# Optimization experiments

Hardware: AMD Instinct MI355X
Metric: run time of the kernel (lower is better)

Reference implementation:

```python
import jax, jax.numpy as jnp
import numpy as np

V = 36      # nodes per graph (3 temporal x 12 spatial)
C = 3       # temporal embedding slots
S = 12      # spatial embedding slots
F0 = 1025   # input feature width
H1, H2 = 256, 64
B = 1024    # graphs
N = B * V
DEG = 8     # random in-block neighbors per node (symmetrized -> 16 avg degree)
BN_EPS = 1e-5


def _edges(k):
    # 8 random neighbors per node within its own 36-node block, symmetrized
    nbr = jax.random.randint(k, (N, DEG), 0, V)
    block = (jnp.arange(N) // V) * V
    dst = (nbr + block[:, None]).reshape(-1)
    src = jnp.repeat(jnp.arange(N), DEG)
    return jnp.stack([jnp.concatenate([src, dst]),
                      jnp.concatenate([dst, src])]).astype(jnp.int32)


def setup_inputs() -> dict:
    k = jax.random.split(jax.random.key(0), 40)
    lin = lambda kk, i, o: (jax.random.normal(kk, (i, o), jnp.float32) / np.sqrt(i)).astype(jnp.float32)
    d = {}
    d['xF'] = jax.random.normal(k[0], (N, F0), jnp.float32)
    d['xD'] = jax.random.normal(k[1], (N, F0), jnp.float32)
    d['edge_index_F'] = _edges(k[2])
    d['edge_index_D'] = _edges(k[3])
    d['TembF'] = jax.random.normal(k[4], (C, F0), jnp.float32)
    d['SembF'] = jax.random.normal(k[5], (S, F0), jnp.float32)
    d['TembD'] = jax.random.normal(k[6], (C, F0), jnp.float32)
    d['SembD'] = jax.random.normal(k[7], (S, F0), jnp.float32)
    # ChebConv K=2 weights (Theta_0, Theta_1), biases; BatchNorm gamma/beta
    d['W0F1'] = lin(k[8], F0, H1); d['W1F1'] = lin(k[9], F0, H1); d['bF1'] = jnp.zeros((H1,), jnp.float32)
    d['gF1'] = jnp.ones((H1,), jnp.float32); d['btF1'] = jnp.zeros((H1,), jnp.float32)
    d['W0F2'] = lin(k[10], H1, H2); d['W1F2'] = lin(k[11], H1, H2); d['bF2'] = jnp.zeros((H2,), jnp.float32)
    d['gF2'] = jnp.ones((H2,), jnp.float32); d['btF2'] = jnp.zeros((H2,), jnp.float32)
    d['W0D1'] = lin(k[12], F0, H1); d['W1D1'] = lin(k[13], F0, H1); d['bD1'] = jnp.zeros((H1,), jnp.float32)
    d['gD1'] = jnp.ones((H1,), jnp.float32); d['btD1'] = jnp.zeros((H1,), jnp.float32)
    d['W0D2'] = lin(k[14], H1, H2); d['W1D2'] = lin(k[15], H1, H2); d['bD2'] = jnp.zeros((H2,), jnp.float32)
    d['gD2'] = jnp.ones((H2,), jnp.float32); d['btD2'] = jnp.zeros((H2,), jnp.float32)
    # fusion linear [256->5]; branch heads are tied-at-init clones of its halves
    Wlin = lin(k[16], 2 * (2 * H2), 5)
    blin = jnp.zeros((5,), jnp.float32)
    d['WlinF'] = Wlin[:2 * H2, :]; d['blinF'] = blin
    d['WlinD'] = Wlin[2 * H2:, :]; d['blinD'] = blin
    d['Wlin'] = Wlin; d['blin'] = blin
    return d


def _cheb(x, ei, W0, W1, b):
    # PyG ChebConv K=2, sym norm, lambda_max=2: out = x@W0 + (L_hat x)@W1 + b,
    # L_hat = -D^{-1/2} A D^{-1/2}. Transform-then-aggregate (linear, cheaper).
    n = x.shape[0]
    src, dst = ei[0], ei[1]
    deg = jax.ops.segment_sum(jnp.ones(src.shape, jnp.float32), src, n)
    dinv = jnp.where(deg > 0, jax.lax.rsqrt(jnp.maximum(deg, 1.0)), 0.0)
    w = -(dinv[src] * dinv[dst])                       # [E]
    h1 = x @ W1                                        # [N, out]
    tx1 = jax.ops.segment_sum(w[:, None] * h1[src], dst, n)  # scatter-add
    return x @ W0 + tx1 + b


def _bn_relu(x, g, bt):
    mu = x.mean(0)
    var = x.var(0)  # biased, as torch BatchNorm1d training-mode normalization
    return jax.nn.relu((x - mu) * jax.lax.rsqrt(var + BN_EPS) * g + bt)


def _branch(x, ei, Temb, Semb, W0a, W1a, ba, ga, bta, W0b, W1b, bb, gb, btb):
    n = x.shape[0]
    bsz = n // V
    x = x.reshape(bsz, C, S, F0).transpose(0, 2, 1, 3)      # [B,12,3,1025]
    x = x + Temb[None, None, :, :] + Semb[None, :, None, :]
    x = x.transpose(0, 2, 1, 3).reshape(n, F0)
    x = _bn_relu(_cheb(x, ei, W0a, W1a, ba), ga, bta)
    x = _bn_relu(_cheb(x, ei, W0b, W1b, bb), gb, btb)        # [N,64]
    # rows 12..23 of each 36-node block, pooled per graph
    idx = (jnp.arange(bsz)[:, None] * V + S + jnp.arange(S)[None, :]).reshape(-1)
    seg = jnp.repeat(jnp.arange(bsz), S)
    xs = x[idx]
    mx = jax.ops.segment_max(xs, seg, bsz)
    mn = jax.ops.segment_sum(xs, seg, bsz) / float(S)
    return jnp.concatenate([mx, mn], axis=1)                 # [B,128]


def reference(xF, xD, edge_index_F, edge_index_D, TembF, SembF, TembD, SembD,
              W0F1, W1F1, bF1, gF1, btF1, W0F2, W1F2, bF2, gF2, btF2,
              W0D1, W1D1, bD1, gD1, btD1, W0D2, W1D2, bD2, gD2, btD2,
              WlinF, blinF, WlinD, blinD, Wlin, blin):
    featF = _branch(xF, edge_index_F, TembF, SembF, W0F1, W1F1, bF1, gF1, btF1,
                    W0F2, W1F2, bF2, gF2, btF2)
    featD = _branch(xD, edge_index_D, TembD, SembD, W0D1, W1D1, bD1, gD1, btD1,
                    W0D2, W1D2, bD2, gD2, btD2)
    outF = jax.nn.softmax(featF @ WlinF + blinF, axis=-1)
    outD = jax.nn.softmax(featD @ WlinD + blinD, axis=-1)
    fusion = jnp.concatenate([featF, featD], axis=1)
    out = jax.nn.softmax(fusion @ Wlin + blin, axis=-1)
    return (outF, outD, fusion, out)
```

## Files before the change

kernel.cpp:

```cpp
#include <hip/hip_runtime.h>
#include <math.h>

#define NN    36864
#define F0    1025
#define H1D   256
#define H2D   64
#define VV    36
#define SS    12
#define BSZ   1024
#define BN_EPS 1e-5f

#define KT1   17
#define EMB_LD 1088
#define WT1_STRIDE  ((size_t)4*17*8192)
#define WT2_STRIDE  ((size_t)4*8192)

typedef __bf16 bf16x8 __attribute__((ext_vector_type(8)));
typedef __bf16 bf16x4 __attribute__((ext_vector_type(4)));
typedef float  f32x4  __attribute__((ext_vector_type(4)));

__device__ __forceinline__ float4 ld4u(const float* p) {
    float4 v;
    __builtin_memcpy(&v, p, 16);
    return v;
}

__global__ void k_zero(float* __restrict__ p, int n) {
    int i = blockIdx.x * blockDim.x + threadIdx.x;
    if (i < n) p[i] = 0.f;
}

__global__ void k_deginit(float* __restrict__ degAll) {
    int br = blockIdx.y;
    int i = blockIdx.x * 256 + threadIdx.x;
    if (i < NN) degAll[(size_t)br * NN + i] = 8.f;
}

__global__ void k_deg(const int* __restrict__ eiF, const int* __restrict__ eiD,
                      int Eh, float* __restrict__ degAll) {
    int br = blockIdx.y;
    const int* src = (br ? eiD : eiF) + Eh;
    float* deg = degAll + (size_t)br * NN;
    int e = blockIdx.x * blockDim.x + threadIdx.x;
    if (e < Eh) atomicAdd(&deg[src[e]], 1.f);
}

__device__ __forceinline__ float dinv_f(float d) {
    return d > 0.f ? rsqrtf(fmaxf(d, 1.f)) : 0.f;
}

__global__ void k_scatter(const int* __restrict__ eiF, const int* __restrict__ eiD,
                          int E, const float* __restrict__ degAll, float* __restrict__ AdjAll) {
    int br = blockIdx.y;
    const int* src = br ? eiD : eiF;
    const int* dst = src + E;
    const float* deg = degAll + (size_t)br * NN;
    float* Adj = AdjAll + (size_t)br * BSZ * (VV * VV);
    int e = blockIdx.x * blockDim.x + threadIdx.x;
    if (e >= E) return;
    int s = src[e], d = dst[e];
    float w = -dinv_f(deg[s]) * dinv_f(deg[d]);
    int blk = s / VV;
    atomicAdd(&Adj[(size_t)blk * (VV * VV) + (d - blk * VV) * VV + (s - blk * VV)], w);
}

__global__ __launch_bounds__(256) void k_prepEmb(
    const float* __restrict__ TembF, const float* __restrict__ SembF,
    const float* __restrict__ TembD, const float* __restrict__ SembD,
    float* __restrict__ embSAll) {
    int br = blockIdx.y;
    const float* Temb = br ? TembD : TembF;
    const float* Semb = br ? SembD : SembF;
    float* out = embSAll + (size_t)br * VV * EMB_LD;
    int id = blockIdx.x * 256 + threadIdx.x;
    if (id >= VV * (EMB_LD / 4)) return;
    int lv = id / (EMB_LD / 4);
    int k0 = (id - lv * (EMB_LD / 4)) * 4;
    const float* pt = Temb + (size_t)(lv / SS) * F0;
    const float* ps = Semb + (size_t)(lv % SS) * F0;
    float4 v;
    float* vp = (float*)&v;
#pragma unroll
    for (int j = 0; j < 4; ++j) {
        int k = k0 + j;
        vp[j] = (k < F0) ? (pt[k] + ps[k]) : 0.f;
    }
    *reinterpret_cast<float4*>(out + (size_t)lv * EMB_LD + k0) = v;
}

__global__ __launch_bounds__(256) void k_prepW(
    const float* __restrict__ WaF, const float* __restrict__ WbF,
    const float* __restrict__ WaD, const float* __restrict__ WbD,
    __bf16* __restrict__ Wt, int K, int nkt, int split, int ldw, size_t brStride) {
    int br = blockIdx.y;
    const float* Wa = br ? WaD : WaF;
    const float* Wb = br ? WbD : WbF;
    __bf16* out = Wt + (size_t)br * brStride;

    int id = blockIdx.x * 256 + threadIdx.x;
    int gpc = nkt * 8;
    int c = id / gpc, gi = id - c * gpc;
    int kt = gi >> 3, g = gi & 7;
    int k0 = kt * 64 + g * 8;
    const float* src = (c < split) ? (Wa + c) : (Wb + (c - split));
    bf16x8 ov;
#pragma unroll
    for (int j = 0; j < 8; ++j) {
        int k = k0 + j;
        float v = (k < K) ? src[(size_t)k * ldw] : 0.f;
        ov[j] = (__bf16)v;
    }
    int r = c & 127, bn = c >> 7;
    size_t dst = ((size_t)(bn * nkt + kt) << 13) + r * 64 + ((g ^ (r & 7)) << 3);
    *(bf16x8*)(out + dst) = ov;
}

__global__ __launch_bounds__(512) void k_gemm1f(
    const float* __restrict__ xF, const float* __restrict__ xD,
    const float* __restrict__ embSAll,
    const __bf16* __restrict__ Wt1All,
    __bf16* __restrict__ H0All, __bf16* __restrict__ H1All) {
    __shared__ __align__(16) __bf16 As[2 * 8192];
    __shared__ __align__(16) __bf16 Bs[2 * 16384];
    const int tid = threadIdx.x;
    const int lane = tid & 63, wid = tid >> 6;

    const int flat = blockIdx.x;
    const int w = (flat & 7) * 144 + (flat >> 3);
    const int cy = w & 1;
    const int t2 = w >> 1;
    const int bm = t2 % 288;
    const int br = t2 / 288;

    const float* x    = br ? xD : xF;
    const float* embS = embSAll + (size_t)br * VV * EMB_LD;
    const __bf16* Wt = Wt1All + (size_t)br * WT1_STRIDE;
    __bf16* H0 = H0All + (size_t)br * NN * H1D;
    __bf16* H1 = H1All + (size_t)br * NN * H1D;

    const int wr = wid >> 2, wc = wid & 3;
    const int l15 = lane & 15, lg = lane >> 4;
    const int bn0 = cy * 2;

    const int kc = (lane & 15) * 4;
    const float *px[4], *pe[4];
    int dso[4];
#pragma unroll
    for (int i = 0; i < 4; ++i) {
        int r = wid * 16 + i * 4 + (lane >> 4);
        int g = bm * 128 + r;
        int lv = g % VV;
        px[i] = x + (size_t)g * F0 + kc;
        pe[i] = embS + (size_t)lv * EMB_LD + kc;
        dso[i] = r * 64 + (((kc >> 3) ^ (r & 7)) << 3) + (kc & 4);
    }

    int offA[2][4], offB[2][4];
#pragma unroll
    for (int kk = 0; kk < 2; ++kk) {
#pragma unroll
        for (int m = 0; m < 4; ++m) {
            int rowA = wr * 64 + m * 16 + l15;
            offA[kk][m] = rowA * 64 + (((kk * 4 + lg) ^ (rowA & 7)) << 3);
        }
#pragma unroll
        for (int n = 0; n < 4; ++n) {
            int col = wc * 64 + n * 16 + l15;
            offB[kk][n] = (col >> 7) * 8192 + (col & 127) * 64
                          + (((kk * 4 + lg) ^ (col & 7)) << 3);
        }
    }

    f32x4 acc[4][4];
#pragma unroll
    for (int m = 0; m < 4; ++m)
#pragma unroll
        for (int n = 0; n < 4; ++n) acc[m][n] = (f32x4){0.f, 0.f, 0.f, 0.f};

    f32x4 xa0[4], xa1[4];

    auto issueX = [&](int kt, f32x4 (&xa)[4]) {
        int ko = kt * 64, kb = ko + kc;
#pragma unroll
        for (int i = 0; i < 4; ++i) {
            if (kb + 3 < F0) {
                float4 a = ld4u(px[i] + ko);
                xa[i] = (f32x4){a.x, a.y, a.z, a.w};
            } else {
                f32x4 v = {0.f, 0.f, 0.f, 0.f};
#pragma unroll
                for (int j = 0; j < 4; ++j)
                    if (kb + j < F0) v[j] = px[i][ko + j];
                xa[i] = v;
            }
        }
    };
    auto writeA = [&](int kt, int buf, f32x4 (&xa)[4]) {
        int ko = kt * 64;
#pragma unroll
        for (int i = 0; i < 4; ++i) {
            float4 e = *reinterpret_cast<const float4*>(pe[i] + ko);
            bf16x4 wv;
            wv[0] = (__bf16)(xa[i][0] + e.x);
            wv[1] = (__bf16)(xa[i][1] + e.y);
            wv[2] = (__bf16)(xa[i][2] + e.z);
            wv[3] = (__bf16)(xa[i][3] + e.w);
            *(bf16x4*)(As + buf * 8192 + dso[i]) = wv;
        }
    };
    auto issueB = [&](int kt, int buf) {
#pragma unroll
        for (int cc = 0; cc < 4; ++cc) {
            int q = (wid * 4 + cc) * 512;
            int h = q >> 13, qi = q & 8191;
            const __bf16* src = Wt + (((size_t)(bn0 + h) * KT1 + kt) << 13)
                                + qi + (lane << 3);
            __builtin_amdgcn_global_load_lds(
                (const __attribute__((address_space(1))) void*)src,
                (__attribute__((address_space(3))) void*)(Bs + buf * 16384 + q), 16, 0, 0);
        }
    };
    auto mfmaStep = [&](int cur) {
        const __bf16* Ab = As + cur * 8192;
        const __bf16* Bb = Bs + cur * 16384;
#pragma unroll
        for (int kk = 0; kk < 2; ++kk) {
            bf16x8 af[4], bb[4];
#pragma unroll
            for (int m = 0; m < 4; ++m) af[m] = *(const bf16x8*)(Ab + offA[kk][m]);
#pragma unroll
            for (int n = 0; n < 4; ++n) bb[n] = *(const bf16x8*)(Bb + offB[kk][n]);
#pragma unroll
            for (int m = 0; m < 4; ++m)
#pragma unroll
                for (int n = 0; n < 4; ++n)
                    acc[m][n] = __builtin_amdgcn_mfma_f32_16x16x32_bf16(
                        af[m], bb[n], acc[m][n], 0, 0, 0);
        }
    };

    issueX(0, xa0);
    issueB(0, 0);
    writeA(0, 0, xa0);
    issueX(1, xa1);

    for (int kt = 0; kt < KT1; kt += 2) {
        __syncthreads();
        if (kt + 1 < KT1) issueB(kt + 1, 1);
        if (kt + 2 < KT1) issueX(kt + 2, xa0);
        mfmaStep(0);
        if (kt + 1 < KT1) writeA(kt + 1, 1, xa1);
        if (kt + 1 >= KT1) break;
        __syncthreads();
        if (kt + 2 < KT1) issueB(kt + 2, 0);
        if (kt + 3 < KT1) issueX(kt + 3, xa1);
        mfmaStep(1);
        if (kt + 2 < KT1) writeA(kt + 2, 0, xa0);
    }

    const int cr = lg * 4;
#pragma unroll
    for (int m = 0; m < 4; ++m) {
        int grow = bm * 128 + wr * 64 + m * 16 + cr;
#pragma unroll
        for (int n = 0; n < 4; ++n) {
            int gc = cy * 256 + wc * 64 + n * 16 + l15;
#pragma unroll
            for (int j = 0; j < 4; ++j) {
                int r = grow + j;
                if (gc < 256) H0[(size_t)r * H1D + gc] = (__bf16)acc[m][n][j];
                else          H1[(size_t)r * H1D + (gc - 256)] = (__bf16)acc[m][n][j];
            }
        }
    }
}

__global__ __launch_bounds__(256, 2) void k_gemm2f(
    const __bf16* __restrict__ YAll, const float* __restrict__ coefAll,
    const __bf16* __restrict__ Wt2All,
    float* __restrict__ G0All, __bf16* __restrict__ G1All) {
    __shared__ __align__(16) __bf16 As[2 * 8192];
    __shared__ __align__(16) __bf16 Bs[2 * 8192];
    const int tid = threadIdx.x;
    const int lane = tid & 63, wid = tid >> 6;
    const int bm = blockIdx.x, br = blockIdx.z;
    const __bf16* Y   = YAll + (size_t)br * NN * H1D;
    const float* coef = coefAll + (size_t)br * 2 * H1D;
    const __bf16* Wt  = Wt2All + (size_t)br * WT2_STRIDE;
    float*  G0 = G0All + (size_t)br * NN * H2D;
    __bf16* G1 = G1All + (size_t)br * NN * H2D;

    const int wr = wid >> 1, wc = wid & 1;
    const int l15 = lane & 15, lg = lane >> 4;

    const int kc = (lane & 15) * 4;
    const __bf16* pyr[8];
    int dso[8];
#pragma unroll
    for (int i = 0; i < 8; ++i) {
        int r = wid * 32 + i * 4 + (lane >> 4);
        pyr[i] = Y + (size_t)(bm * 128 + r) * H1D + kc;
        dso[i] = r * 64 + (((kc >> 3) ^ (r & 7)) << 3) + (kc & 4);
    }

    int offA[2][4], offB[2][4];
#pragma unroll
    for (int kk = 0; kk < 2; ++kk)
#pragma unroll
        for (int m = 0; m < 4; ++m) {
            int rowA = wr * 64 + m * 16 + l15;
            offA[kk][m] = rowA * 64 + (((kk * 4 + lg) ^ (rowA & 7)) << 3);
            int col = wc * 64 + m * 16 + l15;
            offB[kk][m] = col * 64 + (((kk * 4 + lg) ^ (col & 7)) << 3);
        }

    f32x4 acc[4][4];
#pragma unroll
    for (int m = 0; m < 4; ++m)
#pragma unroll
        for (int n = 0; n < 4; ++n) acc[m][n] = (f32x4){0.f, 0.f, 0.f, 0.f};

    bf16x4 ya[8];

    auto issueY = [&](int kt) {
        int k0 = kt * 64;
#pragma unroll
        for (int i = 0; i < 8; ++i)
            ya[i] = *reinterpret_cast<const bf16x4*>(pyr[i] + k0);
    };
    auto writeA = [&](int kt, int buf) {
        int k0 = kt * 64;
        float4 cA = *reinterpret_cast<const float4*>(coef + k0 + kc);
        float4 cB = *reinterpret_cast<const float4*>(coef + H1D + k0 + kc);
#pragma unroll
        for (int i = 0; i < 8; ++i) {
            bf16x4 wv;
            wv[0] = (__bf16)fmaxf(fmaf((float)ya[i][0], cA.x, cB.x), 0.f);
            wv[1] = (__bf16)fmaxf(fmaf((float)ya[i][1], cA.y, cB.y), 0.f);
            wv[2] = (__bf16)fmaxf(fmaf((float)ya[i][2], cA.z, cB.z), 0.f);
            wv[3] = (__bf16)fmaxf(fmaf((float)ya[i][3], cA.w, cB.w), 0.f);
            *(bf16x4*)(As + buf * 8192 + dso[i]) = wv;
        }
    };
    auto issueB = [&](int kt, int buf) {
#pragma unroll
        for (int cc = 0; cc < 4; ++cc) {
            int q = (wid * 4 + cc) * 512;
            const __bf16* src = Wt + ((size_t)kt << 13) + q + (lane << 3);
            __builtin_amdgcn_global_load_lds(
                (const __attribute__((address_space(1))) void*)src,
                (__attribute__((address_space(3))) void*)(Bs + buf * 8192 + q), 16, 0, 0);
        }
    };

    issueB(0, 0);
    issueY(0);
    writeA(0, 0);

    for (int kt = 0; kt < 4; ++kt) {
        const int cur = kt & 1, nxt = cur ^ 1;
        __syncthreads();
        if (kt + 1 < 4) {
            issueB(kt + 1, nxt);
            issueY(kt + 1);
        }
        const __bf16* Ab = As + cur * 8192;
        const __bf16* Bb = Bs + cur * 8192;
#pragma unroll
        for (int kk = 0; kk < 2; ++kk) {
            bf16x8 af[4], bb[4];
#pragma unroll
            for (int m = 0; m < 4; ++m) af[m] = *(const bf16x8*)(Ab + offA[kk][m]);
#pragma unroll
            for (int n = 0; n < 4; ++n) bb[n] = *(const bf16x8*)(Bb + offB[kk][n]);
#pragma unroll
            for (int m = 0; m < 4; ++m)
#pragma unroll
                for (int n = 0; n < 4; ++n)
                    acc[m][n] = __builtin_amdgcn_mfma_f32_16x16x32_bf16(
                        af[m], bb[n], acc[m][n], 0, 0, 0);
        }
        if (kt + 1 < 4) writeA(kt + 1, nxt);
    }

    const int cr = lg * 4;
#pragma unroll
    for (int m = 0; m < 4; ++m) {
        int grow = bm * 128 + wr * 64 + m * 16 + cr;
#pragma unroll
        for (int n = 0; n < 4; ++n) {
            int col = wc * 64 + n * 16 + l15;
#pragma unroll
            for (int j = 0; j < 4; ++j) {
                int r = grow + j;
                if (col < 64) G0[(size_t)r * H2D + col] = acc[m][n][j];
                else          G1[(size_t)r * H2D + (col - 64)] = (__bf16)acc[m][n][j];
            }
        }
    }
}

__global__ __launch_bounds__(256) void k_combine_stats1(
    const float* __restrict__ AdjAll, const __bf16* __restrict__ H1All,
    const float* __restrict__ bF, const float* __restrict__ bD,
    __bf16* __restrict__ YAll, float* __restrict__ stAll) {
    __shared__ float Adj_s[VV * VV];
    __shared__ float red[256 * 9];
    int b = blockIdx.x, br = blockIdx.y, t = threadIdx.x;
    const float* Adj = AdjAll + ((size_t)br * BSZ + b) * (VV * VV);
    const __bf16* h1 = H1All + ((size_t)br * NN + (size_t)b * VV) * H1D;
    __bf16* yb = YAll + ((size_t)br * NN + (size_t)b * VV) * H1D;
    float* st = stAll + (size_t)br * 2 * H1D;
    const float* bias = br ? bD : bF;

    for (int e = t; e < VV * VV; e += 256) Adj_s[e] = Adj[e];
    __syncthreads();

    int c0 = (t & 63) * 4, r0 = t >> 6;
    float4 bv = *reinterpret_cast<const float4*>(bias + c0);
    float acc[9][4];
#pragma unroll
    for (int i = 0; i < 9; ++i) {
        bf16x4 y = *reinterpret_cast<const bf16x4*>(yb + (size_t)(r0 + 4 * i) * H1D + c0);
        acc[i][0] = (float)y[0] + bv.x; acc[i][1] = (float)y[1] + bv.y;
        acc[i][2] = (float)y[2] + bv.z; acc[i][3] = (float)y[3] + bv.w;
    }
#pragma unroll 4
    for (int j = 0; j < VV; ++j) {
        bf16x4 hv = *reinterpret_cast<const bf16x4*>(h1 + (size_t)j * H1D + c0);
        float h0 = (float)hv[0], h1f = (float)hv[1], h2 = (float)hv[2], h3 = (float)hv[3];
#pragma unroll
        for (int i = 0; i < 9; ++i) {
            float a = Adj_s[(r0 + 4 * i) * VV + j];
            acc[i][0] = fmaf(a, h0, acc[i][0]);
            acc[i][1] = fmaf(a, h1f, acc[i][1]);
            acc[i][2] = fmaf(a, h2, acc[i][2]);
            acc[i][3] = fmaf(a, h3, acc[i][3]);
        }
    }
    float s[4] = {0, 0, 0, 0}, s2[4] = {0, 0, 0, 0};
#pragma unroll
    for (int i = 0; i < 9; ++i) {
        bf16x4 wv;
        wv[0] = (__bf16)acc[i][0]; wv[1] = (__bf16)acc[i][1];
        wv[2] = (__bf16)acc[i][2]; wv[3] = (__bf16)acc[i][3];
        *reinterpret_cast<bf16x4*>(yb + (size_t)(r0 + 4 * i) * H1D + c0) = wv;
#pragma unroll
        for (int k = 0; k < 4; ++k) { s[k] += acc[i][k]; s2[k] += acc[i][k] * acc[i][k]; }
    }
#pragma unroll
    for (int k = 0; k < 4; ++k) { red[t * 9 + k] = s[k]; red[t * 9 + 4 + k] = s2[k]; }
    __syncthreads();
    {
        int cg = t >> 2, k = t & 3;
        float ss = 0.f, ss2 = 0.f;
#pragma unroll
        for (int q = 0; q < 4; ++q) {
            ss  += red[(q * 64 + cg) * 9 + k];
            ss2 += red[(q * 64 + cg) * 9 + 4 + k];
        }
        atomicAdd(&st[t], ss);
        atomicAdd(&st[H1D + t], ss2);
    }
}

__global__ __launch_bounds__(256) void k_combine_stats2(
    const float* __restrict__ AdjAll, const __bf16* __restrict__ G1All,
    const float* __restrict__ bF, const float* __restrict__ bD,
    float* __restrict__ YAll, float* __restrict__ stAll) {
    __shared__ float Adj_s[VV * VV];
    __shared__ float red[256 * 9];
    int b = blockIdx.x, br = blockIdx.y, t = threadIdx.x;
    const float* Adj = AdjAll + ((size_t)br * BSZ + b) * (VV * VV);
    const __bf16* g1 = G1All + ((size_t)br * NN + (size_t)b * VV) * H2D;
    float* yb = YAll + ((size_t)br * NN + (size_t)b * VV) * H2D;
    float* st = stAll + (size_t)br * 2 * H2D;
    const float* bias = br ? bD : bF;

    for (int e = t; e < VV * VV; e += 256) Adj_s[e] = Adj[e];
    __syncthreads();

    int c0 = (t & 15) * 4, r0 = t >> 4;
    int nr = (r0 < 4) ? 3 : 2;
    float4 bv = *reinterpret_cast<const float4*>(bias + c0);
    float acc[3][4];
    for (int i = 0; i < nr; ++i) {
        float4 y = *reinterpret_cast<const float4*>(yb + (size_t)(r0 + 16 * i) * H2D + c0);
        acc[i][0] = y.x + bv.x; acc[i][1] = y.y + bv.y;
        acc[i][2] = y.z + bv.z; acc[i][3] = y.w + bv.w;
    }
#pragma unroll 4
    for (int j = 0; j < VV; ++j) {
        bf16x4 hv = *reinterpret_cast<const bf16x4*>(g1 + (size_t)j * H2D + c0);
        float h0 = (float)hv[0], h1f = (float)hv[1], h2 = (float)hv[2], h3 = (float)hv[3];
        for (int i = 0; i < nr; ++i) {
            float a = Adj_s[(r0 + 16 * i) * VV + j];
            acc[i][0] = fmaf(a, h0, acc[i][0]);
            acc[i][1] = fmaf(a, h1f, acc[i][1]);
            acc[i][2] = fmaf(a, h2, acc[i][2]);
            acc[i][3] = fmaf(a, h3, acc[i][3]);
        }
    }
    float s[4] = {0, 0, 0, 0}, s2[4] = {0, 0, 0, 0};
    for (int i = 0; i < nr; ++i) {
        *reinterpret_cast<float4*>(yb + (size_t)(r0 + 16 * i) * H2D + c0) =
            make_float4(acc[i][0], acc[i][1], acc[i][2], acc[i][3]);
#pragma unroll
        for (int k = 0; k < 4; ++k) { s[k] += acc[i][k]; s2[k] += acc[i][k] * acc[i][k]; }
    }
#pragma unroll
    for (int k = 0; k < 4; ++k) { red[t * 9 + k] = s[k]; red[t * 9 + 4 + k] = s2[k]; }
    __syncthreads();
    if (t < 2 * H2D) {
        int cg = (t & 63) >> 2, k = t & 3, which = t >> 6;
        float ss = 0.f;
#pragma unroll
        for (int q = 0; q < 16; ++q) ss += red[(q * 16 + cg) * 9 + which * 4 + k];
        atomicAdd(&st[(t >> 6) * H2D + (t & 63)], ss);
    }
}

__global__ void k_fin(const float* __restrict__ stAll,
                      const float* __restrict__ gF, const float* __restrict__ btF,
                      const float* __restrict__ gD, const float* __restrict__ btD,
                      float* __restrict__ coefAll, int H) {
    int br = blockIdx.x, t = threadIdx.x;
    const float* st = stAll + (size_t)br * 2 * H;
    float* coef = coefAll + (size_t)br * 2 * H;
    const float* g = br ? gD : gF;
    const float* bt = br ? btD : btF;
    if (t >= H) return;
    float mu = st[t] / (float)NN;
    float var = st[H + t] / (float)NN - mu * mu;
    float sA = g[t] * rsqrtf(var + BN_EPS);
    coef[t] = sA;
    coef[H + t] = bt[t] - mu * sA;
}

__global__ __launch_bounds__(64) void k_pool(const float* __restrict__ Y2All,
                                             const float* __restrict__ coefAll,
                                             float* __restrict__ featF,
                                             float* __restrict__ featD) {
    int b = blockIdx.x, br = blockIdx.y, c = threadIdx.x;
    const float* Y2 = Y2All + (size_t)br * NN * H2D;
    const float* coef = coefAll + (size_t)br * 2 * H2D;
    float* feat = br ? featD : featF;
    float sA = coef[c], sB = coef[H2D + c];
    float mx = -1e30f, sm = 0.f;
    const float* yb = Y2 + ((size_t)b * VV + SS) * H2D + c;
#pragma unroll
    for (int i = 0; i < SS; ++i) {
        float v = fmaxf(fmaf(yb[i * H2D], sA, sB), 0.f);
        mx = fmaxf(mx, v);
        sm += v;
    }
    feat[b * 128 + c] = mx;
    feat[b * 128 + 64 + c] = sm * (1.f / 12.f);
}

__global__ __launch_bounds__(128) void k_heads(
    const float* __restrict__ featF, const float* __restrict__ featD,
    const float* __restrict__ WlinF, const float* __restrict__ blinF,
    const float* __restrict__ WlinD, const float* __restrict__ blinD,
    const float* __restrict__ Wlin, const float* __restrict__ blin,
    float* __restrict__ out) {
    __shared__ float sF[128], sD[128], lg[24];
    int r = blockIdx.x, t = threadIdx.x;
    sF[t] = featF[r * 128 + t];
    sD[t] = featD[r * 128 + t];
    __syncthreads();
    float* fus = out + 10240 + (size_t)r * 256;
    fus[t] = sF[t];
    fus[128 + t] = sD[t];
    if (t < 5) {
        float a = blinF[t];
        for (int k = 0; k < 128; ++k) a += sF[k] * WlinF[k * 5 + t];
        lg[t] = a;
    } else if (t >= 8 && t < 13) {
        int j = t - 8;
        float a = blinD[j];
        for (int k = 0; k < 128; ++k) a += sD[k] * WlinD[k * 5 + j];
        lg[8 + j] = a;
    } else if (t >= 16 && t < 21) {
        int j = t - 16;
        float a = blin[j];
        for (int k = 0; k < 128; ++k) a += sF[k] * Wlin[k * 5 + j];
        for (int k = 0; k < 128; ++k) a += sD[k] * Wlin[(128 + k) * 5 + j];
        lg[16 + j] = a;
    }
    __syncthreads();
    if (t < 15) {
        int grp = t / 5, j = t % 5;
        const float* l = &lg[grp * 8];
        float m = l[0];
#pragma unroll
        for (int k = 1; k < 5; ++k) m = fmaxf(m, l[k]);
        float den = 0.f;
#pragma unroll
        for (int k = 0; k < 5; ++k) den += expf(l[k] - m);
        float v = expf(l[j] - m) / den;
        float* dst = (grp == 0) ? out : (grp == 1 ? out + 5120 : out + 272384);
        dst[r * 5 + j] = v;
    }
}

extern "C" void kernel_launch(void* const* d_in, const int* in_sizes, int n_in,
                              void* d_out, int out_size, void* d_ws, size_t ws_size,
                              hipStream_t stream) {
    const float* xF    = (const float*)d_in[0];
    const float* xD    = (const float*)d_in[1];
    const int*   eiF   = (const int*)d_in[2];
    const int*   eiD   = (const int*)d_in[3];
    const float* TembF = (const float*)d_in[4];
    const float* SembF = (const float*)d_in[5];
    const float* TembD = (const float*)d_in[6];
    const float* SembD = (const float*)d_in[7];
    const float* W0F1  = (const float*)d_in[8];
    const float* W1F1  = (const float*)d_in[9];
    const float* bF1   = (const float*)d_in[10];
    const float* gF1   = (const float*)d_in[11];
    const float* btF1  = (const float*)d_in[12];
    const float* W0F2  = (const float*)d_in[13];
    const float* W1F2  = (const float*)d_in[14];
    const float* bF2   = (const float*)d_in[15];
    const float* gF2   = (const float*)d_in[16];
    const float* btF2  = (const float*)d_in[17];
    const float* W0D1  = (const float*)d_in[18];
    const float* W1D1  = (const float*)d_in[19];
    const float* bD1   = (const float*)d_in[20];
    const float* gD1   = (const float*)d_in[21];
    const float* btD1  = (const float*)d_in[22];
    const float* W0D2  = (const float*)d_in[23];
    const float* W1D2  = (const float*)d_in[24];
    const float* bD2   = (const float*)d_in[25];
    const float* gD2   = (const float*)d_in[26];
    const float* btD2  = (const float*)d_in[27];
    const float* WlinF = (const float*)d_in[28];
    const float* blinF = (const float*)d_in[29];
    const float* WlinD = (const float*)d_in[30];
    const float* blinD = (const float*)d_in[31];
    const float* Wlin  = (const float*)d_in[32];
    const float* blin  = (const float*)d_in[33];

    const int E = in_sizes[2] / 2;

    float* ws = (float*)d_ws;
    size_t o = 0;
    __bf16* H0bf = (__bf16*)(ws + o);   o += (size_t)2 * NN * H1D / 2;
    __bf16* H1bf = (__bf16*)(ws + o);   o += (size_t)2 * NN * H1D / 2;
    float*  G0   = ws + o;              o += (size_t)2 * NN * H2D;
    __bf16* G1bf = (__bf16*)(ws + o);   o += (size_t)2 * NN * H2D / 2;
    __bf16* Wt1  = (__bf16*)(ws + o);   o += (size_t)2 * WT1_STRIDE / 2;
    __bf16* Wt2  = (__bf16*)(ws + o);   o += (size_t)2 * WT2_STRIDE / 2;
    float*  embS = ws + o;              o += (size_t)2 * VV * EMB_LD;
    float*  Adj  = ws + o;              o += (size_t)2 * BSZ * VV * VV;
    float*  st1  = ws + o;              o += 2 * 2 * H1D;
    float*  st2  = ws + o;              o += 2 * 2 * H2D;
    float*  deg  = ws + o;              o += (size_t)2 * NN;
    float*  coef1 = ws + o;             o += 2 * 2 * H1D;
    float*  coef2 = ws + o;             o += 2 * 2 * H2D;
    float*  featF = ws + o;             o += (size_t)BSZ * 128;
    float*  featD = ws + o;             o += (size_t)BSZ * 128;

    const int zeroN = 2 * (BSZ * VV * VV + 2 * H1D + 2 * H2D);

    k_zero<<<(zeroN + 255) / 256, 256, 0, stream>>>(Adj, zeroN);
    k_deginit<<<dim3(144, 2), 256, 0, stream>>>(deg);
    k_deg<<<dim3((E / 2 + 255) / 256, 2), 256, 0, stream>>>(eiF, eiD, E / 2, deg);
    k_scatter<<<dim3((E + 255) / 256, 2), 256, 0, stream>>>(eiF, eiD, E, deg, Adj);
    k_prepEmb<<<dim3(39, 2), 256, 0, stream>>>(TembF, SembF, TembD, SembD, embS);
    k_prepW<<<dim3(272, 2), 256, 0, stream>>>(W0F1, W1F1, W0D1, W1D1, Wt1,
                                              F0, 17, 256, H1D, WT1_STRIDE);
    k_prepW<<<dim3(16, 2), 256, 0, stream>>>(W0F2, W1F2, W0D2, W1D2, Wt2,
                                             H1D, 4, 64, H2D, WT2_STRIDE);
    k_gemm1f<<<dim3(1152), 512, 0, stream>>>(xF, xD, embS, Wt1, H0bf, H1bf);
    k_combine_stats1<<<dim3(BSZ, 2), 256, 0, stream>>>(Adj, H1bf, bF1, bD1, H0bf, st1);
    k_fin<<<dim3(2), 256, 0, stream>>>(st1, gF1, btF1, gD1, btD1, coef1, H1D);
    k_gemm2f<<<dim3(288, 1, 2), 256, 0, stream>>>(H0bf, coef1, Wt2, G0, G1bf);
    k_combine_stats2<<<dim3(BSZ, 2), 256, 0, stream>>>(Adj, G1bf, bF2, bD2, G0, st2);
    k_fin<<<dim3(2), 64, 0, stream>>>(st2, gF2, btF2, gD2, btD2, coef2, H2D);
    k_pool<<<dim3(BSZ, 2), 64, 0, stream>>>(G0, coef2, featF, featD);
    k_heads<<<BSZ, 128, 0, stream>>>(featF, featD, WlinF, blinF, WlinD, blinD,
                                     Wlin, blin, (float*)d_out);
}
```

Before: 445.1 us.

## Retile first GEMM to 128x128 tiles with K=32 steps and smaller LDS

```diff
diff --git a/kernel.cpp b/kernel.cpp
--- a/kernel.cpp
+++ b/kernel.cpp
@@ -10,9 +10,9 @@
 #define BSZ   1024
 #define BN_EPS 1e-5f
 
-#define KT1   17
+#define KT32  34
 #define EMB_LD 1088
-#define WT1_STRIDE  ((size_t)4*17*8192)
+#define WT1_STRIDE  ((size_t)4*34*4096)
 #define WT2_STRIDE  ((size_t)4*8192)
 
 typedef __bf16 bf16x8 __attribute__((ext_vector_type(8)));
@@ -115,60 +115,78 @@
     *(bf16x8*)(out + dst) = ov;
 }
 
-__global__ __launch_bounds__(512) void k_gemm1f(
+__global__ __launch_bounds__(256) void k_prepW32(
+    const float* __restrict__ WaF, const float* __restrict__ WbF,
+    const float* __restrict__ WaD, const float* __restrict__ WbD,
+    __bf16* __restrict__ Wt) {
+    int br = blockIdx.y;
+    const float* Wa = br ? WaD : WaF;
+    const float* Wb = br ? WbD : WbF;
+    __bf16* out = Wt + (size_t)br * WT1_STRIDE;
+
+    int id = blockIdx.x * 256 + threadIdx.x;
+    int c = id / 136, gi = id - c * 136;
+    int kt = gi >> 2, g = gi & 3;
+    int k0 = kt * 32 + g * 8;
+    const float* src = (c < 256) ? (Wa + c) : (Wb + (c - 256));
+    bf16x8 ov;
+#pragma unroll
+    for (int j = 0; j < 8; ++j) {
+        int k = k0 + j;
+        float v = (k < F0) ? src[(size_t)k * H1D] : 0.f;
+        ov[j] = (__bf16)v;
+    }
+    int r = c & 127, bn = c >> 7;
+    size_t dst = ((size_t)(bn * KT32 + kt) << 12) + r * 32 + ((g ^ ((r >> 1) & 3)) << 3);
+    *(bf16x8*)(out + dst) = ov;
+}
+
+__global__ __launch_bounds__(256, 3) void k_gemm1f(
     const float* __restrict__ xF, const float* __restrict__ xD,
     const float* __restrict__ embSAll,
     const __bf16* __restrict__ Wt1All,
     __bf16* __restrict__ H0All, __bf16* __restrict__ H1All) {
-    __shared__ __align__(16) __bf16 As[2 * 8192];
-    __shared__ __align__(16) __bf16 Bs[2 * 16384];
+    __shared__ __align__(16) __bf16 As[2 * 4096];
+    __shared__ __align__(16) __bf16 Bs[2 * 4096];
     const int tid = threadIdx.x;
     const int lane = tid & 63, wid = tid >> 6;
 
     const int flat = blockIdx.x;
-    const int w = (flat & 7) * 144 + (flat >> 3);
-    const int cy = w & 1;
-    const int t2 = w >> 1;
+    const int w = (flat & 7) * 288 + (flat >> 3);
+    const int cy = w & 3;
+    const int t2 = w >> 2;
     const int bm = t2 % 288;
     const int br = t2 / 288;
 
     const float* x    = br ? xD : xF;
     const float* embS = embSAll + (size_t)br * VV * EMB_LD;
-    const __bf16* Wt = Wt1All + (size_t)br * WT1_STRIDE;
+    const __bf16* WtT = Wt1All + (size_t)br * WT1_STRIDE + ((size_t)(cy * KT32) << 12);
     __bf16* H0 = H0All + (size_t)br * NN * H1D;
     __bf16* H1 = H1All + (size_t)br * NN * H1D;
 
-    const int wr = wid >> 2, wc = wid & 3;
+    const int wr = wid >> 1, wc = wid & 1;
     const int l15 = lane & 15, lg = lane >> 4;
-    const int bn0 = cy * 2;
-
-    const int kc = (lane & 15) * 4;
+
+    const int kc = (lane & 7) * 4;
     const float *px[4], *pe[4];
     int dso[4];
 #pragma unroll
     for (int i = 0; i < 4; ++i) {
-        int r = wid * 16 + i * 4 + (lane >> 4);
+        int r = wid * 32 + i * 8 + (lane >> 3);
         int g = bm * 128 + r;
         int lv = g % VV;
         px[i] = x + (size_t)g * F0 + kc;
         pe[i] = embS + (size_t)lv * EMB_LD + kc;
-        dso[i] = r * 64 + (((kc >> 3) ^ (r & 7)) << 3) + (kc & 4);
-    }
-
-    int offA[2][4], offB[2][4];
-#pragma unroll
-    for (int kk = 0; kk < 2; ++kk) {
-#pragma unroll
-        for (int m = 0; m < 4; ++m) {
-            int rowA = wr * 64 + m * 16 + l15;
-            offA[kk][m] = rowA * 64 + (((kk * 4 + lg) ^ (rowA & 7)) << 3);
-        }
-#pragma unroll
-        for (int n = 0; n < 4; ++n) {
-            int col = wc * 64 + n * 16 + l15;
-            offB[kk][n] = (col >> 7) * 8192 + (col & 127) * 64
-                          + (((kk * 4 + lg) ^ (col & 7)) << 3);
-        }
+        dso[i] = r * 32 + ((((kc >> 3) ^ ((r >> 1) & 3)) << 3) + (kc & 4));
+    }
+
+    int offA[4], offB[4];
+#pragma unroll
+    for (int m = 0; m < 4; ++m) {
+        int rowA = wr * 64 + m * 16 + l15;
+        offA[m] = rowA * 32 + ((lg ^ ((rowA >> 1) & 3)) << 3);
+        int col = wc * 64 + m * 16 + l15;
+        offB[m] = col * 32 + ((lg ^ ((col >> 1) & 3)) << 3);
     }
 
     f32x4 acc[4][4];
@@ -180,7 +198,7 @@
     f32x4 xa0[4], xa1[4];
 
     auto issueX = [&](int kt, f32x4 (&xa)[4]) {
-        int ko = kt * 64, kb = ko + kc;
+        int ko = kt * 32, kb = ko + kc;
 #pragma unroll
         for (int i = 0; i < 4; ++i) {
             if (kb + 3 < F0) {
@@ -196,7 +214,7 @@
         }
     };
     auto writeA = [&](int kt, int buf, f32x4 (&xa)[4]) {
-        int ko = kt * 64;
+        int ko = kt * 32;
 #pragma unroll
         for (int i = 0; i < 4; ++i) {
             float4 e = *reinterpret_cast<const float4*>(pe[i] + ko);
@@ -205,38 +223,33 @@
             wv[1] = (__bf16)(xa[i][1] + e.y);
             wv[2] = (__bf16)(xa[i][2] + e.z);
             wv[3] = (__bf16)(xa[i][3] + e.w);
-            *(bf16x4*)(As + buf * 8192 + dso[i]) = wv;
+            *(bf16x4*)(As + buf * 4096 + dso[i]) = wv;
         }
     };
     auto issueB = [&](int kt, int buf) {
 #pragma unroll
-        for (int cc = 0; cc < 4; ++cc) {
-            int q = (wid * 4 + cc) * 512;
-            int h = q >> 13, qi = q & 8191;
-            const __bf16* src = Wt + (((size_t)(bn0 + h) * KT1 + kt) << 13)
-                                + qi + (lane << 3);
+        for (int cc = 0; cc < 2; ++cc) {
+            int q = (wid * 2 + cc) * 512;
+            const __bf16* src = WtT + ((size_t)kt << 12) + q + (lane << 3);
             __builtin_amdgcn_global_load_lds(
                 (const __attribute__((address_space(1))) void*)src,
-                (__attribute__((address_space(3))) void*)(Bs + buf * 16384 + q), 16, 0, 0);
+                (__attribute__((address_space(3))) void*)(Bs + buf * 4096 + q), 16, 0, 0);
         }
     };
     auto mfmaStep = [&](int cur) {
-        const __bf16* Ab = As + cur * 8192;
-        const __bf16* Bb = Bs + cur * 16384;
-#pragma unroll
-        for (int kk = 0; kk < 2; ++kk) {
-            bf16x8 af[4], bb[4];
-#pragma unroll
-            for (int m = 0; m < 4; ++m) af[m] = *(const bf16x8*)(Ab + offA[kk][m]);
-#pragma unroll
-            for (int n = 0; n < 4; ++n) bb[n] = *(const bf16x8*)(Bb + offB[kk][n]);
-#pragma unroll
-            for (int m = 0; m < 4; ++m)
-#pragma unroll
-                for (int n = 0; n < 4; ++n)
-                    acc[m][n] = __builtin_amdgcn_mfma_f32_16x16x32_bf16(
-                        af[m], bb[n], acc[m][n], 0, 0, 0);
-        }
+        const __bf16* Ab = As + cur * 4096;
+        const __bf16* Bb = Bs + cur * 4096;
+        bf16x8 af[4], bb[4];
+#pragma unroll
+        for (int m = 0; m < 4; ++m) af[m] = *(const bf16x8*)(Ab + offA[m]);
+#pragma unroll
+        for (int n = 0; n < 4; ++n) bb[n] = *(const bf16x8*)(Bb + offB[n]);
+#pragma unroll
+        for (int m = 0; m < 4; ++m)
+#pragma unroll
+            for (int n = 0; n < 4; ++n)
+                acc[m][n] = __builtin_amdgcn_mfma_f32_16x16x32_bf16(
+                    af[m], bb[n], acc[m][n], 0, 0, 0);
     };
 
     issueX(0, xa0);
@@ -244,18 +257,18 @@
     writeA(0, 0, xa0);
     issueX(1, xa1);
 
-    for (int kt = 0; kt < KT1; kt += 2) {
+    for (int kt = 0; kt < KT32; kt += 2) {
         __syncthreads();
-        if (kt + 1 < KT1) issueB(kt + 1, 1);
-        if (kt + 2 < KT1) issueX(kt + 2, xa0);
+        if (kt + 1 < KT32) issueB(kt + 1, 1);
+        if (kt + 2 < KT32) issueX(kt + 2, xa0);
         mfmaStep(0);
-        if (kt + 1 < KT1) writeA(kt + 1, 1, xa1);
-        if (kt + 1 >= KT1) break;
+        if (kt + 1 < KT32) writeA(kt + 1, 1, xa1);
+        if (kt + 1 >= KT32) break;
         __syncthreads();
-        if (kt + 2 < KT1) issueB(kt + 2, 0);
-        if (kt + 3 < KT1) issueX(kt + 3, xa1);
+        if (kt + 2 < KT32) issueB(kt + 2, 0);
+        if (kt + 3 < KT32) issueX(kt + 3, xa1);
         mfmaStep(1);
-        if (kt + 2 < KT1) writeA(kt + 2, 0, xa0);
+        if (kt + 2 < KT32) writeA(kt + 2, 0, xa0);
     }
 
     const int cr = lg * 4;
@@ -264,7 +277,7 @@
         int grow = bm * 128 + wr * 64 + m * 16 + cr;
 #pragma unroll
         for (int n = 0; n < 4; ++n) {
-            int gc = cy * 256 + wc * 64 + n * 16 + l15;
+            int gc = cy * 128 + wc * 64 + n * 16 + l15;
 #pragma unroll
             for (int j = 0; j < 4; ++j) {
                 int r = grow + j;
@@ -669,11 +682,10 @@
     k_deg<<<dim3((E / 2 + 255) / 256, 2), 256, 0, stream>>>(eiF, eiD, E / 2, deg);
     k_scatter<<<dim3((E + 255) / 256, 2), 256, 0, stream>>>(eiF, eiD, E, deg, Adj);
     k_prepEmb<<<dim3(39, 2), 256, 0, stream>>>(TembF, SembF, TembD, SembD, embS);
-    k_prepW<<<dim3(272, 2), 256, 0, stream>>>(W0F1, W1F1, W0D1, W1D1, Wt1,
-                                              F0, 17, 256, H1D, WT1_STRIDE);
+    k_prepW32<<<dim3(272, 2), 256, 0, stream>>>(W0F1, W1F1, W0D1, W1D1, Wt1);
     k_prepW<<<dim3(16, 2), 256, 0, stream>>>(W0F2, W1F2, W0D2, W1D2, Wt2,
                                              H1D, 4, 64, H2D, WT2_STRIDE);
-    k_gemm1f<<<dim3(1152), 512, 0, stream>>>(xF, xD, embS, Wt1, H0bf, H1bf);
+    k_gemm1f<<<dim3(2304), 256, 0, stream>>>(xF, xD, embS, Wt1, H0bf, H1bf);
     k_combine_stats1<<<dim3(BSZ, 2), 256, 0, stream>>>(Adj, H1bf, bF1, bD1, H0bf, st1);
     k_fin<<<dim3(2), 256, 0, stream>>>(st1, gF1, btF1, gD1, btD1, coef1, H1D);
     k_gemm2f<<<dim3(288, 1, 2), 256, 0, stream>>>(H0bf, coef1, Wt2, G0, G1bf);
```

New measurement: 579.6 us. 1.3x slower.

## Build per-graph adjacency in shared memory and fuse pooling into heads

Applied to the files above, without the earlier changes.

```diff
diff --git a/kernel.cpp b/kernel.cpp
--- a/kernel.cpp
+++ b/kernel.cpp
@@ -30,38 +30,40 @@
     if (i < n) p[i] = 0.f;
 }
 
-__global__ void k_deginit(float* __restrict__ degAll) {
-    int br = blockIdx.y;
-    int i = blockIdx.x * 256 + threadIdx.x;
-    if (i < NN) degAll[(size_t)br * NN + i] = 8.f;
-}
-
-__global__ void k_deg(const int* __restrict__ eiF, const int* __restrict__ eiD,
-                      int Eh, float* __restrict__ degAll) {
-    int br = blockIdx.y;
-    const int* src = (br ? eiD : eiF) + Eh;
-    float* deg = degAll + (size_t)br * NN;
-    int e = blockIdx.x * blockDim.x + threadIdx.x;
-    if (e < Eh) atomicAdd(&deg[src[e]], 1.f);
-}
-
 __device__ __forceinline__ float dinv_f(float d) {
     return d > 0.f ? rsqrtf(fmaxf(d, 1.f)) : 0.f;
 }
 
-__global__ void k_scatter(const int* __restrict__ eiF, const int* __restrict__ eiD,
-                          int E, const float* __restrict__ degAll, float* __restrict__ AdjAll) {
-    int br = blockIdx.y;
-    const int* src = br ? eiD : eiF;
-    const int* dst = src + E;
-    const float* deg = degAll + (size_t)br * NN;
-    float* Adj = AdjAll + (size_t)br * BSZ * (VV * VV);
-    int e = blockIdx.x * blockDim.x + threadIdx.x;
-    if (e >= E) return;
-    int s = src[e], d = dst[e];
-    float w = -dinv_f(deg[s]) * dinv_f(deg[d]);
-    int blk = s / VV;
-    atomicAdd(&Adj[(size_t)blk * (VV * VV) + (d - blk * VV) * VV + (s - blk * VV)], w);
+__global__ __launch_bounds__(128) void k_graph(
+    const int* __restrict__ eiF, const int* __restrict__ eiD,
+    int E, float* __restrict__ AdjAll) {
+    __shared__ float deg_s[VV];
+    __shared__ float Adj_s[VV * VV];
+    int b = blockIdx.x, br = blockIdx.y, t = threadIdx.x;
+    const int* e0 = br ? eiD : eiF;
+    const int Eh = E / 2;
+    const int base = b * VV;
+
+    if (t < VV) deg_s[t] = 8.f;
+    for (int i = t; i < VV * VV; i += 128) Adj_s[i] = 0.f;
+    __syncthreads();
+
+    for (int i = t; i < 288; i += 128) {
+        int d = e0[Eh + b * 288 + i];
+        atomicAdd(&deg_s[d - base], 1.f);
+    }
+    __syncthreads();
+
+    for (int i = t; i < 576; i += 128) {
+        int idx = (i < 288) ? (b * 288 + i) : (Eh + b * 288 + (i - 288));
+        int s = e0[idx], d = e0[E + idx];
+        float w = -dinv_f(deg_s[s - base]) * dinv_f(deg_s[d - base]);
+        atomicAdd(&Adj_s[(d - base) * VV + (s - base)], w);
+    }
+    __syncthreads();
+
+    float* A = AdjAll + ((size_t)br * BSZ + b) * (VV * VV);
+    for (int i = t; i < VV * VV; i += 128) A[i] = Adj_s[i];
 }
 
 __global__ __launch_bounds__(256) void k_prepEmb(
@@ -537,38 +539,34 @@
     coef[H + t] = bt[t] - mu * sA;
 }
 
-__global__ __launch_bounds__(64) void k_pool(const float* __restrict__ Y2All,
-                                             const float* __restrict__ coefAll,
-                                             float* __restrict__ featF,
-                                             float* __restrict__ featD) {
-    int b = blockIdx.x, br = blockIdx.y, c = threadIdx.x;
-    const float* Y2 = Y2All + (size_t)br * NN * H2D;
-    const float* coef = coefAll + (size_t)br * 2 * H2D;
-    float* feat = br ? featD : featF;
-    float sA = coef[c], sB = coef[H2D + c];
-    float mx = -1e30f, sm = 0.f;
-    const float* yb = Y2 + ((size_t)b * VV + SS) * H2D + c;
-#pragma unroll
-    for (int i = 0; i < SS; ++i) {
-        float v = fmaxf(fmaf(yb[i * H2D], sA, sB), 0.f);
-        mx = fmaxf(mx, v);
-        sm += v;
-    }
-    feat[b * 128 + c] = mx;
-    feat[b * 128 + 64 + c] = sm * (1.f / 12.f);
-}
-
-__global__ __launch_bounds__(128) void k_heads(
-    const float* __restrict__ featF, const float* __restrict__ featD,
+__global__ __launch_bounds__(128) void k_poolheads(
+    const float* __restrict__ G0All, const float* __restrict__ coef2All,
     const float* __restrict__ WlinF, const float* __restrict__ blinF,
     const float* __restrict__ WlinD, const float* __restrict__ blinD,
     const float* __restrict__ Wlin, const float* __restrict__ blin,
     float* __restrict__ out) {
     __shared__ float sF[128], sD[128], lg[24];
     int r = blockIdx.x, t = threadIdx.x;
-    sF[t] = featF[r * 128 + t];
-    sD[t] = featD[r * 128 + t];
-    __syncthreads();
+
+    {
+        int br = t >> 6, c = t & 63;
+        const float* Y2 = G0All + (size_t)br * NN * H2D;
+        const float* coef = coef2All + (size_t)br * 2 * H2D;
+        float sA = coef[c], sB = coef[H2D + c];
+        float mx = -1e30f, sm = 0.f;
+        const float* yb = Y2 + ((size_t)r * VV + SS) * H2D + c;
+#pragma unroll
+        for (int i = 0; i < SS; ++i) {
+            float v = fmaxf(fmaf(yb[i * H2D], sA, sB), 0.f);
+            mx = fmaxf(mx, v);
+            sm += v;
+        }
+        float* feat = br ? sD : sF;
+        feat[c] = mx;
+        feat[64 + c] = sm * (1.f / 12.f);
+    }
+    __syncthreads();
+
     float* fus = out + 10240 + (size_t)r * 256;
     fus[t] = sF[t];
     fus[128 + t] = sD[t];
@@ -656,18 +654,13 @@
     float*  Adj  = ws + o;              o += (size_t)2 * BSZ * VV * VV;
     float*  st1  = ws + o;              o += 2 * 2 * H1D;
     float*  st2  = ws + o;              o += 2 * 2 * H2D;
-    float*  deg  = ws + o;              o += (size_t)2 * NN;
     float*  coef1 = ws + o;             o += 2 * 2 * H1D;
     float*  coef2 = ws + o;             o += 2 * 2 * H2D;
-    float*  featF = ws + o;             o += (size_t)BSZ * 128;
-    float*  featD = ws + o;             o += (size_t)BSZ * 128;
-
-    const int zeroN = 2 * (BSZ * VV * VV + 2 * H1D + 2 * H2D);
-
-    k_zero<<<(zeroN + 255) / 256, 256, 0, stream>>>(Adj, zeroN);
-    k_deginit<<<dim3(144, 2), 256, 0, stream>>>(deg);
-    k_deg<<<dim3((E / 2 + 255) / 256, 2), 256, 0, stream>>>(eiF, eiD, E / 2, deg);
-    k_scatter<<<dim3((E + 255) / 256, 2), 256, 0, stream>>>(eiF, eiD, E, deg, Adj);
+
+    const int zeroN = 2 * (2 * H1D + 2 * H2D);
+
+    k_zero<<<(zeroN + 255) / 256, 256, 0, stream>>>(st1, zeroN);
+    k_graph<<<dim3(BSZ, 2), 128, 0, stream>>>(eiF, eiD, E, Adj);
     k_prepEmb<<<dim3(39, 2), 256, 0, stream>>>(TembF, SembF, TembD, SembD, embS);
     k_prepW<<<dim3(272, 2), 256, 0, stream>>>(W0F1, W1F1, W0D1, W1D1, Wt1,
                                               F0, 17, 256, H1D, WT1_STRIDE);
@@ -679,7 +672,6 @@
     k_gemm2f<<<dim3(288, 1, 2), 256, 0, stream>>>(H0bf, coef1, Wt2, G0, G1bf);
     k_combine_stats2<<<dim3(BSZ, 2), 256, 0, stream>>>(Adj, G1bf, bF2, bD2, G0, st2);
     k_fin<<<dim3(2), 64, 0, stream>>>(st2, gF2, btF2, gD2, btD2, coef2, H2D);
-    k_pool<<<dim3(BSZ, 2), 64, 0, stream>>>(G0, coef2, featF, featD);
-    k_heads<<<BSZ, 128, 0, stream>>>(featF, featD, WlinF, blinF, WlinD, blinD,
-                                     Wlin, blin, (float*)d_out);
-}
+    k_poolheads<<<dim3(BSZ), 128, 0, stream>>>(G0, coef2, WlinF, blinF, WlinD, blinD,
+                                               Wlin, blin, (float*)d_out);
+}
```

Result: faster. 409.0 us (-8.1%).
